# Kernel tuning notes

Hardware: AMD Instinct MI355X
Metric: run time of the kernel (lower is better)

## Reference

```python
import jax, jax.numpy as jnp
import numpy as np

B = 512; H = 84; W = 84; K = 20; DEPTH = 24; EMB = 512
FCS = 7 * 7 * 64
FLOW_C = 0.01


def _init(key, shape, fan_in):
    return jax.random.normal(key, shape, jnp.float32) * (1.0 / np.sqrt(fan_in))


def setup_inputs() -> dict:
    key = jax.random.key(0)
    ks = jax.random.split(key, 22)
    return {
        "inp": jax.random.normal(ks[0], (B, 2, H, W), jnp.float32),
        "cw1": _init(ks[1], (32, 2, 8, 8), 2 * 8 * 8),
        "cb1": jnp.zeros((32,), jnp.float32),
        "cw2": _init(ks[2], (64, 32, 4, 4), 32 * 4 * 4),
        "cb2": jnp.zeros((64,), jnp.float32),
        "cw3": _init(ks[3], (64, 64, 3, 3), 64 * 3 * 3),
        "cb3": jnp.zeros((64,), jnp.float32),
        "fcw": _init(ks[4], (EMB, FCS), FCS),
        "fcb": jnp.zeros((EMB,), jnp.float32),
        "otw": _init(ks[5], (K * 2, EMB), EMB),
        "otb": jnp.zeros((K * 2,), jnp.float32),
        "ctw": _init(ks[6], (2, EMB), EMB),
        "ctb": jnp.zeros((2,), jnp.float32),
        "m1w": _init(ks[7], (21 * 21 * DEPTH, EMB), EMB),
        "m1b": jnp.zeros((21 * 21 * DEPTH,), jnp.float32),
        "c1w": _init(ks[8], (DEPTH, DEPTH, 3, 3), DEPTH * 9),
        "c1b": jnp.zeros((DEPTH,), jnp.float32),
        "c2w": _init(ks[9], (DEPTH, DEPTH, 3, 3), DEPTH * 9),
        "c2b": jnp.zeros((DEPTH,), jnp.float32),
        "c3w": _init(ks[10], (K, DEPTH, 1, 1), DEPTH),
        "c3b": jnp.zeros((K,), jnp.float32),
    }


def _conv(x, w, b, stride, pad):
    y = jax.lax.conv_general_dilated(
        x, w, (stride, stride), [(pad, pad), (pad, pad)],
        dimension_numbers=("NCHW", "OIHW", "NCHW"))
    return y + b[None, :, None, None]


def _up_mat(in_s, out_s):
    # bilinear, align_corners=True (torch UpsamplingBilinear2d)
    pos = jnp.arange(out_s, dtype=jnp.float32) * ((in_s - 1) / (out_s - 1))
    lo = jnp.clip(jnp.floor(pos).astype(jnp.int32), 0, in_s - 2)
    w = pos - lo.astype(jnp.float32)
    r = jnp.arange(out_s)
    M = jnp.zeros((out_s, in_s), jnp.float32)
    M = M.at[r, lo].add(1.0 - w).at[r, lo + 1].add(w)
    return M


def reference(inp, cw1, cb1, cw2, cb2, cw3, cb3, fcw, fcb, otw, otb,
              ctw, ctb, m1w, m1b, c1w, c1b, c2w, c2b, c3w, c3b):
    bs = inp.shape[0]
    # CNN encoder
    h1 = jax.nn.relu(_conv(inp, cw1, cb1, 4, 0))
    h2 = jax.nn.relu(_conv(h1, cw2, cb2, 2, 0))
    h3 = jax.nn.relu(_conv(h2, cw3, cb3, 1, 0))
    feat = h3.reshape(bs, -1)                              # [B, 3136]
    x = jax.nn.relu(feat @ fcw.T + fcb)                    # [B, EMB]
    # mask decoder
    m = (x @ m1w.T + m1b).reshape(bs, DEPTH, 21, 21)
    M42 = _up_mat(21, 42)
    m = jnp.einsum('bchw,Hh,Ww->bcHW', m, M42, M42)        # 21->42
    m = jax.nn.relu(m + _conv(m, c1w, c1b, 1, 1))
    M84 = _up_mat(42, 84)
    m = jnp.einsum('bchw,Hh,Ww->bcHW', m, M84, M84)        # 42->84
    m = jax.nn.relu(m + _conv(m, c2w, c2b, 1, 1))
    m = jax.nn.sigmoid(_conv(m, c3w, c3b, 1, 0))           # [B, K, 84, 84]
    # per-object translations -> flow
    ot = (x @ otw.T + otb).reshape(bs, K, 2)
    flow = jnp.einsum('bkhw,bkt->bthw', m, ot).reshape(bs, 2, H * W)
    ct = (x @ ctw.T + ctb)[:, :, None]                     # [B,2,1]
    flat_flow = flow + ct
    img_size_f = FLOW_C * jnp.array([[float(H)], [float(W)]], jnp.float32)
    # mesh grid: row 0 = y (row index), row 1 = x (col index)
    gy = jnp.repeat(jnp.arange(H, dtype=jnp.float32), W)
    gx = jnp.tile(jnp.arange(W, dtype=jnp.float32), H)
    grid = jnp.stack([gy, gx], 0)                          # [2, H*W]
    coords = img_size_f * flat_flow + grid
    ys = coords[:, 0, :].reshape(-1)                       # [B*H*W]
    xs = coords[:, 1, :].reshape(-1)
    # manual bilinear gather from second input frame
    src = inp[:, 1, :, :].reshape(-1)                      # [B*H*W] flat image
    x0 = jnp.clip(jnp.floor(xs).astype(jnp.int32), 0, W - 1)
    x1 = jnp.clip(x0 + 1, 0, W - 1)
    y0 = jnp.clip(jnp.floor(ys).astype(jnp.int32), 0, H - 1)
    y1 = jnp.clip(y0 + 1, 0, H - 1)
    base = jnp.repeat(jnp.arange(bs, dtype=jnp.int32) * (H * W), H * W)
    Ia = src[base + y0 * W + x0]
    Ib = src[base + y1 * W + x0]
    Ic = src[base + y0 * W + x1]
    Id = src[base + y1 * W + x1]
    xc = jnp.clip(xs, 0.0, float(W - 1))
    yc = jnp.clip(ys, 0.0, float(H - 1))
    x0f = x0.astype(jnp.float32); x1f = x1.astype(jnp.float32)
    y0f = y0.astype(jnp.float32); y1f = y1.astype(jnp.float32)
    out = ((x1f - xc) * (y1f - yc) * Ia + (x1f - xc) * (yc - y0f) * Ib +
           (xc - x0f) * (y1f - yc) * Ic + (xc - x0f) * (yc - y0f) * Id)
    return out.reshape(bs, 1, H, W)
```

## Files before the change

kernel.cpp:

```cpp
#include <hip/hip_runtime.h>
#include <math.h>

namespace {

typedef float f32x2 __attribute__((ext_vector_type(2)));

#if defined(__has_builtin)
#if __has_builtin(__builtin_elementwise_fma)
#define HAVE_EW_FMA 1
#endif
#endif

__device__ __forceinline__ f32x2 pkfma(f32x2 a, f32x2 b, f32x2 c) {
#ifdef HAVE_EW_FMA
  return __builtin_elementwise_fma(a, b, c);
#else
  return a * b + c;
#endif
}

constexpr int IMS  = 84;
constexpr int NPIX = IMS * IMS;
constexpr int KOBJ = 20;

constexpr size_t OFF_X    = 0;
constexpr size_t OFF_OT   = 262144;
constexpr size_t OFF_CT   = 282624;
constexpr size_t OFF_WT2  = 283648;
constexpr size_t OFF_WT3  = 316416;
constexpr size_t OFF_M0   = 353280;
constexpr size_t OFF_R1   = 5772288;
constexpr size_t OFF_H1   = OFF_R1;
constexpr size_t OFF_H2   = 12325888;
constexpr size_t OFF_FEAT = 14980096;

__global__ void transpose_w(const float* __restrict__ w, float* __restrict__ wt,
                            int OC, int CKK) {
  int idx = blockIdx.x * 256 + threadIdx.x;
  if (idx < OC * CKK) {
    int oc = idx / CKK, ckk = idx % CKK;
    wt[ckk * OC + oc] = w[idx];
  }
}

__global__ __launch_bounds__(256) void conv1_k(
    const float* __restrict__ inp, const float* __restrict__ w,
    const float* __restrict__ bias, float* __restrict__ out) {
  __shared__ __align__(16) float sIn[NPIX];
  __shared__ __align__(16) float sW[128 * 32];
  const int b = blockIdx.x, t = threadIdx.x;
  for (int i = t; i < 4096; i += 256) {
    int oc = i >> 7, ckk = i & 127;
    sW[ckk * 32 + oc] = w[i];
  }
  const float* ip = inp + (size_t)b * 2 * NPIX;
  const int oc0 = (t & 7) * 4;
  const int pg  = t >> 3;
  int ibase[13];
#pragma unroll
  for (int k = 0; k < 13; k++) {
    int p = pg + 32 * k; if (p > 399) p = 399;
    ibase[k] = (p / 20) * 4 * 84 + (p % 20) * 4;
  }
  f32x2 acc[13][2];
#pragma unroll
  for (int k = 0; k < 13; k++) { acc[k][0] = f32x2{0.f, 0.f}; acc[k][1] = f32x2{0.f, 0.f}; }
  for (int c = 0; c < 2; c++) {
    __syncthreads();
    for (int i = t; i < NPIX; i += 256) sIn[i] = ip[c * NPIX + i];
    __syncthreads();
    for (int u = 0; u < 8; u++) {
#pragma unroll
      for (int v = 0; v < 8; v++) {
        const float4 wv = *(const float4*)&sW[((c * 8 + u) * 8 + v) * 32 + oc0];
        const f32x2 w0 = {wv.x, wv.y}, w1 = {wv.z, wv.w};
        const int off = u * 84 + v;
#pragma unroll
        for (int k = 0; k < 13; k++) {
          float x = sIn[off + ibase[k]];
          f32x2 xv = {x, x};
          acc[k][0] = pkfma(w0, xv, acc[k][0]);
          acc[k][1] = pkfma(w1, xv, acc[k][1]);
        }
      }
    }
  }
  float b0 = bias[oc0], b1 = bias[oc0+1], b2 = bias[oc0+2], b3 = bias[oc0+3];
  float* op = out + (size_t)b * 32 * 400;
#pragma unroll
  for (int k = 0; k < 13; k++) {
    int p = pg + 32 * k;
    if (p < 400) {
      op[(oc0+0)*400 + p] = fmaxf(acc[k][0][0] + b0, 0.f);
      op[(oc0+1)*400 + p] = fmaxf(acc[k][0][1] + b1, 0.f);
      op[(oc0+2)*400 + p] = fmaxf(acc[k][1][0] + b2, 0.f);
      op[(oc0+3)*400 + p] = fmaxf(acc[k][1][1] + b3, 0.f);
    }
  }
}

__global__ __launch_bounds__(256) void conv2_k(
    const float* __restrict__ in, const float* __restrict__ wt,
    const float* __restrict__ bias, float* __restrict__ out) {
  __shared__ float sIn[32 * 400];
  const int b = blockIdx.x, t = threadIdx.x;
  const float* ip = in + (size_t)b * 12800;
  for (int i = t; i < 12800; i += 256) sIn[i] = ip[i];
  __syncthreads();
  const int oc0 = (t & 7) * 8;
  const int pg  = t >> 3;
  int base[3];
#pragma unroll
  for (int k = 0; k < 3; k++) {
    int p = pg + 32 * k; if (p > 80) p = 80;
    base[k] = (p / 9) * 40 + (p % 9) * 2;
  }
  f32x2 acc[3][4];
#pragma unroll
  for (int k = 0; k < 3; k++)
#pragma unroll
    for (int o = 0; o < 4; o++) acc[k][o] = f32x2{0.f, 0.f};
  for (int c = 0; c < 32; c++) {
#pragma unroll
    for (int u = 0; u < 4; u++)
#pragma unroll
      for (int v = 0; v < 4; v++) {
        const float* wp = wt + ((c * 4 + u) * 4 + v) * 64 + oc0;
        float4 wa = *(const float4*)wp;
        float4 wb = *(const float4*)(wp + 4);
        const f32x2 w0 = {wa.x, wa.y}, w1 = {wa.z, wa.w};
        const f32x2 w2 = {wb.x, wb.y}, w3 = {wb.z, wb.w};
        int off = c * 400 + u * 20 + v;
#pragma unroll
        for (int k = 0; k < 3; k++) {
          float x = sIn[off + base[k]];
          f32x2 xv = {x, x};
          acc[k][0] = pkfma(w0, xv, acc[k][0]);
          acc[k][1] = pkfma(w1, xv, acc[k][1]);
          acc[k][2] = pkfma(w2, xv, acc[k][2]);
          acc[k][3] = pkfma(w3, xv, acc[k][3]);
        }
      }
  }
  float* op = out + (size_t)b * 5184;
#pragma unroll
  for (int k = 0; k < 3; k++) {
    int p = pg + 32 * k;
    if (p < 81) {
#pragma unroll
      for (int o = 0; o < 8; o++)
        op[(oc0+o)*81 + p] = fmaxf(acc[k][o >> 1][o & 1] + bias[oc0+o], 0.f);
    }
  }
}

__global__ __launch_bounds__(256) void conv3_k(
    const float* __restrict__ in, const float* __restrict__ wt,
    const float* __restrict__ bias, float* __restrict__ out) {
  __shared__ float sIn[64 * 81];
  const int b = blockIdx.x, t = threadIdx.x;
  const float* ip = in + (size_t)b * 5184;
  for (int i = t; i < 5184; i += 256) sIn[i] = ip[i];
  __syncthreads();
  const int oc0 = (t & 7) * 8;
  const int pg  = t >> 3;
  int base[2];
#pragma unroll
  for (int k = 0; k < 2; k++) {
    int p = pg + 32 * k; if (p > 48) p = 48;
    base[k] = (p / 7) * 9 + (p % 7);
  }
  f32x2 acc[2][4];
#pragma unroll
  for (int k = 0; k < 2; k++)
#pragma unroll
    for (int o = 0; o < 4; o++) acc[k][o] = f32x2{0.f, 0.f};
  for (int c = 0; c < 64; c++) {
#pragma unroll
    for (int u = 0; u < 3; u++)
#pragma unroll
      for (int v = 0; v < 3; v++) {
        const float* wp = wt + ((c * 3 + u) * 3 + v) * 64 + oc0;
        float4 wa = *(const float4*)wp;
        float4 wb = *(const float4*)(wp + 4);
        const f32x2 w0 = {wa.x, wa.y}, w1 = {wa.z, wa.w};
        const f32x2 w2 = {wb.x, wb.y}, w3 = {wb.z, wb.w};
        int off = c * 81 + u * 9 + v;
#pragma unroll
        for (int k = 0; k < 2; k++) {
          float x = sIn[off + base[k]];
          f32x2 xv = {x, x};
          acc[k][0] = pkfma(w0, xv, acc[k][0]);
          acc[k][1] = pkfma(w1, xv, acc[k][1]);
          acc[k][2] = pkfma(w2, xv, acc[k][2]);
          acc[k][3] = pkfma(w3, xv, acc[k][3]);
        }
      }
  }
  float* op = out + (size_t)b * 3136;
#pragma unroll
  for (int k = 0; k < 2; k++) {
    int p = pg + 32 * k;
    if (p < 49) {
#pragma unroll
      for (int o = 0; o < 8; o++)
        op[(oc0+o)*49 + p] = fmaxf(acc[k][o >> 1][o & 1] + bias[oc0+o], 0.f);
    }
  }
}

template<bool RELU>
__global__ __launch_bounds__(256) void gemm_k(
    const float* __restrict__ A, const float* __restrict__ Wm,
    const float* __restrict__ bias, float* __restrict__ C,
    int N, int K) {
  __shared__ __align__(16) float As[16][68];
  __shared__ __align__(16) float Ws[16][68];
  const int t = threadIdx.x;
  const int m0 = blockIdx.y * 64, n0 = blockIdx.x * 64;
  const int r  = t >> 2;
  const int kq = (t & 3) * 4;
  const int r0 = (t >> 4) * 4, c0 = (t & 15) * 4;
  f32x2 acc[4][2];
#pragma unroll
  for (int i = 0; i < 4; i++) { acc[i][0] = f32x2{0.f, 0.f}; acc[i][1] = f32x2{0.f, 0.f}; }
  for (int k0 = 0; k0 < K; k0 += 16) {
    float4 a = *(const float4*)(A + (size_t)(m0 + r) * K + k0 + kq);
    int wrow = n0 + r;
    float4 wv = make_float4(0.f, 0.f, 0.f, 0.f);
    if (wrow < N) wv = *(const float4*)(Wm + (size_t)wrow * K + k0 + kq);
    __syncthreads();
    As[kq+0][r] = a.x; As[kq+1][r] = a.y; As[kq+2][r] = a.z; As[kq+3][r] = a.w;
    Ws[kq+0][r] = wv.x; Ws[kq+1][r] = wv.y; Ws[kq+2][r] = wv.z; Ws[kq+3][r] = wv.w;
    __syncthreads();
#pragma unroll
    for (int kk = 0; kk < 16; kk++) {
      float4 av = *(const float4*)&As[kk][r0];
      float4 bv = *(const float4*)&Ws[kk][c0];
      const f32x2 b0 = {bv.x, bv.y}, b1 = {bv.z, bv.w};
      float ar[4] = {av.x, av.y, av.z, av.w};
#pragma unroll
      for (int i = 0; i < 4; i++) {
        f32x2 ai = {ar[i], ar[i]};
        acc[i][0] = pkfma(b0, ai, acc[i][0]);
        acc[i][1] = pkfma(b1, ai, acc[i][1]);
      }
    }
  }
#pragma unroll
  for (int i = 0; i < 4; i++) {
    int row = m0 + r0 + i;
#pragma unroll
    for (int j = 0; j < 4; j++) {
      int col = n0 + c0 + j;
      if (col < N) {
        float v = acc[i][j >> 1][j & 1] + bias[col];
        C[(size_t)row * N + col] = RELU ? fmaxf(v, 0.f) : v;
      }
    }
  }
}

__global__ __launch_bounds__(256, 4) void upconv1_k(
    const float* __restrict__ X, const float* __restrict__ wt,
    const float* __restrict__ bias, float* __restrict__ out) {
  constexpr int S_IN = 21, S_OUT = 42, TR = 6, UH = 8, UW = 44, NTILE = 7;
  __shared__ __align__(16) float sU[24 * UH * UW];
  const int b = blockIdx.x / NTILE;
  const int y0 = (blockIdx.x % NTILE) * TR;
  const int t = threadIdx.x;
  const float* xb = X + (size_t)b * 24 * S_IN * S_IN;
  const float sc = (float)(S_IN - 1) / (float)(S_OUT - 1);
  for (int rr = t; rr < UH * UW; rr += 256) {
    const int ry = rr / UW, cx = rr % UW;
    const int y = y0 + ry - 1, x = cx - 1;
    float* sdst = &sU[rr];
    if (y >= 0 && y < S_OUT && x >= 0 && x < S_OUT) {
      float py = y * sc, px = x * sc;
      int ly = (int)py; if (ly > S_IN - 2) ly = S_IN - 2;
      int lx = (int)px; if (lx > S_IN - 2) lx = S_IN - 2;
      float wy = py - (float)ly, wx = px - (float)lx;
      const f32x2 wxv = {wx, wx};
      const float* xc = xb + ly * S_IN + lx;
      for (int c = 0; c < 24; c++) {
        f32x2 a  = {xc[0], xc[S_IN]};
        f32x2 bb = {xc[1], xc[S_IN + 1]};
        f32x2 h = pkfma(wxv, bb - a, a);
        *sdst = h[0] + wy * (h[1] - h[0]);
        xc += S_IN * S_IN;
        sdst += UH * UW;
      }
    } else {
      for (int c = 0; c < 24; c++) { *sdst = 0.f; sdst += UH * UW; }
    }
  }
  __syncthreads();
  if (t < 252) {
    const int ry = t / 42, lx = t % 42;
    f32x2 acc[12];
#pragma unroll
    for (int j = 0; j < 12; j++) acc[j] = f32x2{0.f, 0.f};
    for (int ic = 0; ic < 24; ic++) {
      const float* urow = &sU[(ic * UH + ry) * UW + lx];
      const float* wp = wt + ic * 216;
#pragma unroll
      for (int ky = 0; ky < 3; ky++) {
        float x0v = urow[ky * UW + 0];
        float x1v = urow[ky * UW + 1];
        float x2v = urow[ky * UW + 2];
        f32x2 X0 = {x0v, x0v}, X1 = {x1v, x1v}, X2 = {x2v, x2v};
        const f32x2* wk2 = (const f32x2*)(wp + ky * 72);
#pragma unroll
        for (int j = 0; j < 12; j++)
          acc[j] = pkfma(wk2[j], X0,
                   pkfma(wk2[12 + j], X1,
                   pkfma(wk2[24 + j], X2, acc[j])));
      }
    }
    const int yy = y0 + ry;
#pragma unroll
    for (int j = 0; j < 12; j++) {
      f32x2 u2 = { sU[((2*j)   * UH + ry + 1) * UW + lx + 1],
                   sU[((2*j+1) * UH + ry + 1) * UW + lx + 1] };
      f32x2 b2 = *(const f32x2*)&bias[2*j];
      f32x2 s = u2 + acc[j] + b2;
      out[(((size_t)b * 24 + 2*j    ) * S_OUT + yy) * S_OUT + lx] = fmaxf(s[0], 0.f);
      out[(((size_t)b * 24 + 2*j + 1) * S_OUT + yy) * S_OUT + lx] = fmaxf(s[1], 0.f);
    }
  }
}

__global__ __launch_bounds__(256, 4) void upconv2_final_k(
    const float* __restrict__ R1, const float* __restrict__ inp,
    const float* __restrict__ wt, const float* __restrict__ bias,
    const float* __restrict__ c3w, const float* __restrict__ c3b,
    const float* __restrict__ ot, const float* __restrict__ ct,
    float* __restrict__ out) {
  constexpr int S_IN = 42, S_OUT = 84, TR = 6, UH = 8, TW = 42, UW = 44;
  __shared__ __align__(16) float sU[24 * UH * UW];
  const int blk = blockIdx.x;
  const int b = blk / 28;
  const int rr0 = blk % 28;
  const int y0 = (rr0 >> 1) * TR;
  const int x0 = (rr0 & 1) * TW;
  const int t = threadIdx.x;
  const float* xb = R1 + (size_t)b * 24 * S_IN * S_IN;
  const float sc = (float)(S_IN - 1) / (float)(S_OUT - 1);
  for (int rr = t; rr < UH * UW; rr += 256) {
    const int ry = rr / UW, cx = rr % UW;
    const int y = y0 + ry - 1, x = x0 + cx - 1;
    float* sdst = &sU[rr];
    if (y >= 0 && y < S_OUT && x >= 0 && x < S_OUT) {
      float py = y * sc, px = x * sc;
      int ly = (int)py; if (ly > S_IN - 2) ly = S_IN - 2;
      int lx = (int)px; if (lx > S_IN - 2) lx = S_IN - 2;
      float wy = py - (float)ly, wx = px - (float)lx;
      const f32x2 wxv = {wx, wx};
      const float* xc = xb + ly * S_IN + lx;
      for (int c = 0; c < 24; c++) {
        f32x2 a  = {xc[0], xc[S_IN]};
        f32x2 bb = {xc[1], xc[S_IN + 1]};
        f32x2 h = pkfma(wxv, bb - a, a);
        *sdst = h[0] + wy * (h[1] - h[0]);
        xc += S_IN * S_IN;
        sdst += UH * UW;
      }
    } else {
      for (int c = 0; c < 24; c++) { *sdst = 0.f; sdst += UH * UW; }
    }
  }
  __syncthreads();
  if (t < 252) {
    const int ry = t / 42, lx = t % 42;
    f32x2 acc[12];
#pragma unroll
    for (int j = 0; j < 12; j++) acc[j] = f32x2{0.f, 0.f};
    for (int ic = 0; ic < 24; ic++) {
      const float* urow = &sU[(ic * UH + ry) * UW + lx];
      const float* wp = wt + ic * 216;
#pragma unroll
      for (int ky = 0; ky < 3; ky++) {
        float x0v = urow[ky * UW + 0];
        float x1v = urow[ky * UW + 1];
        float x2v = urow[ky * UW + 2];
        f32x2 X0 = {x0v, x0v}, X1 = {x1v, x1v}, X2 = {x2v, x2v};
        const f32x2* wk2 = (const f32x2*)(wp + ky * 72);
#pragma unroll
        for (int j = 0; j < 12; j++)
          acc[j] = pkfma(wk2[j], X0,
                   pkfma(wk2[12 + j], X1,
                   pkfma(wk2[24 + j], X2, acc[j])));
      }
    }
    f32x2 r[12];
#pragma unroll
    for (int j = 0; j < 12; j++) {
      f32x2 u2 = { sU[((2*j)   * UH + ry + 1) * UW + lx + 1],
                   sU[((2*j+1) * UH + ry + 1) * UW + lx + 1] };
      f32x2 b2 = *(const f32x2*)&bias[2*j];
      f32x2 s = u2 + acc[j] + b2;
      r[j][0] = fmaxf(s[0], 0.f);
      r[j][1] = fmaxf(s[1], 0.f);
    }
    f32x2 f2 = *(const f32x2*)&ct[b * 2];
    const f32x2* ot2 = (const f32x2*)(ot + b * 2 * KOBJ);
    for (int k = 0; k < KOBJ; k++) {
      f32x2 zv = {c3b[k], 0.f};
      const f32x2* cw2 = (const f32x2*)(c3w + k * 24);
#pragma unroll
      for (int j = 0; j < 12; j++) zv = pkfma(r[j], cw2[j], zv);
      float z = zv[0] + zv[1];
      float m = 1.f / (1.f + __expf(-z));
      f32x2 mv = {m, m};
      f2 = pkfma(mv, ot2[k], f2);
    }
    const int gy = y0 + ry, gx = x0 + lx;
    const float imgf = 0.01f * 84.0f;
    float ys = imgf * f2[0] + (float)gy;
    float xs = imgf * f2[1] + (float)gx;
    int ix0 = (int)floorf(xs); ix0 = ix0 < 0 ? 0 : (ix0 > 83 ? 83 : ix0);
    int iy0 = (int)floorf(ys); iy0 = iy0 < 0 ? 0 : (iy0 > 83 ? 83 : iy0);
    int ix1 = ix0 + 1 > 83 ? 83 : ix0 + 1;
    int iy1 = iy0 + 1 > 83 ? 83 : iy0 + 1;
    float xc = fminf(fmaxf(xs, 0.f), 83.f);
    float yc = fminf(fmaxf(ys, 0.f), 83.f);
    float wx1 = (float)ix1 - xc, wx0 = xc - (float)ix0;
    float wy1 = (float)iy1 - yc, wy0 = yc - (float)iy0;
    const float* src = inp + ((size_t)b * 2 + 1) * NPIX;
    float Ia = src[iy0 * 84 + ix0], Ib = src[iy1 * 84 + ix0];
    float Ic = src[iy0 * 84 + ix1], Id = src[iy1 * 84 + ix1];
    out[(size_t)b * NPIX + gy * 84 + gx] =
        wx1 * wy1 * Ia + wx1 * wy0 * Ib + wx0 * wy1 * Ic + wx0 * wy0 * Id;
  }
}

}

extern "C" void kernel_launch(void* const* d_in, const int* in_sizes, int n_in,
                              void* d_out, int out_size, void* d_ws, size_t ws_size,
                              hipStream_t stream) {
  const float* inp = (const float*)d_in[0];
  const float* cw1 = (const float*)d_in[1];
  const float* cb1 = (const float*)d_in[2];
  const float* cw2 = (const float*)d_in[3];
  const float* cb2 = (const float*)d_in[4];
  const float* cw3 = (const float*)d_in[5];
  const float* cb3 = (const float*)d_in[6];
  const float* fcw = (const float*)d_in[7];
  const float* fcb = (const float*)d_in[8];
  const float* otw = (const float*)d_in[9];
  const float* otb = (const float*)d_in[10];
  const float* ctw = (const float*)d_in[11];
  const float* ctb = (const float*)d_in[12];
  const float* m1w = (const float*)d_in[13];
  const float* m1b = (const float*)d_in[14];
  const float* c1w = (const float*)d_in[15];
  const float* c1b = (const float*)d_in[16];
  const float* c2w = (const float*)d_in[17];
  const float* c2b = (const float*)d_in[18];
  const float* c3w = (const float*)d_in[19];
  const float* c3b = (const float*)d_in[20];
  float* W = (float*)d_ws;
  float* out = (float*)d_out;

  transpose_w<<<(64 * 512 + 255) / 256, 256, 0, stream>>>(cw2, W + OFF_WT2, 64, 512);
  transpose_w<<<(64 * 576 + 255) / 256, 256, 0, stream>>>(cw3, W + OFF_WT3, 64, 576);
  conv1_k<<<512, 256, 0, stream>>>(inp, cw1, cb1, W + OFF_H1);
  conv2_k<<<512, 256, 0, stream>>>(W + OFF_H1, W + OFF_WT2, cb2, W + OFF_H2);
  conv3_k<<<512, 256, 0, stream>>>(W + OFF_H2, W + OFF_WT3, cb3, W + OFF_FEAT);
  transpose_w<<<(24 * 216 + 255) / 256, 256, 0, stream>>>(c1w, W + OFF_WT2, 24, 216);
  transpose_w<<<(24 * 216 + 255) / 256, 256, 0, stream>>>(c2w, W + OFF_WT3, 24, 216);
  gemm_k<true><<<dim3(8, 8), 256, 0, stream>>>(W + OFF_FEAT, fcw, fcb, W + OFF_X, 512, 3136);
  gemm_k<false><<<dim3(1, 8), 256, 0, stream>>>(W + OFF_X, otw, otb, W + OFF_OT, 40, 512);
  gemm_k<false><<<dim3(1, 8), 256, 0, stream>>>(W + OFF_X, ctw, ctb, W + OFF_CT, 2, 512);
  gemm_k<false><<<dim3(166, 8), 256, 0, stream>>>(W + OFF_X, m1w, m1b, W + OFF_M0, 10584, 512);
  upconv1_k<<<512 * 7, 256, 0, stream>>>(W + OFF_M0, W + OFF_WT2, c1b, W + OFF_R1);
  upconv2_final_k<<<512 * 28, 256, 0, stream>>>(W + OFF_R1, inp, W + OFF_WT3, c2b,
                                                c3w, c3b, W + OFF_OT, W + OFF_CT, out);
}
```

Baseline: 1.204 ms.

## Use channel-interleaved shared layout in decoder convs and a 128x128 GEMM tile

```diff
diff --git a/kernel.cpp b/kernel.cpp
--- a/kernel.cpp
+++ b/kernel.cpp
@@ -40,6 +40,14 @@
   if (idx < OC * CKK) {
     int oc = idx / CKK, ckk = idx % CKK;
     wt[ckk * OC + oc] = w[idx];
+  }
+}
+
+__global__ void transpose_dec(const float* __restrict__ w, float* __restrict__ wt) {
+  int idx = blockIdx.x * 256 + threadIdx.x;
+  if (idx < 5184) {
+    int oc = idx / 216, rem = idx % 216, ic = rem / 9, tap = rem % 9;
+    wt[(tap * 24 + ic) * 24 + oc] = w[idx];
   }
 }
 
@@ -261,11 +269,73 @@
   }
 }
 
+__global__ __launch_bounds__(256) void gemm128_k(
+    const float* __restrict__ A, const float* __restrict__ Wm,
+    const float* __restrict__ bias, float* __restrict__ C,
+    int N, int K) {
+  __shared__ __align__(16) float As[16][132];
+  __shared__ __align__(16) float Ws[16][132];
+  const int t = threadIdx.x;
+  const int m0 = blockIdx.y * 128, n0 = blockIdx.x * 128;
+  const int lr = t >> 1;
+  const int kq = (t & 1) * 8;
+  const int r0 = (t >> 4) * 8, c0 = (t & 15) * 8;
+  f32x2 acc[8][4];
+#pragma unroll
+  for (int i = 0; i < 8; i++)
+#pragma unroll
+    for (int j = 0; j < 4; j++) acc[i][j] = f32x2{0.f, 0.f};
+  for (int k0 = 0; k0 < K; k0 += 16) {
+    const float* ap = A + (size_t)(m0 + lr) * K + k0 + kq;
+    float4 a0 = *(const float4*)ap;
+    float4 a1 = *(const float4*)(ap + 4);
+    int wrow = n0 + lr;
+    float4 w0 = make_float4(0.f,0.f,0.f,0.f), w1 = make_float4(0.f,0.f,0.f,0.f);
+    if (wrow < N) {
+      const float* wp = Wm + (size_t)wrow * K + k0 + kq;
+      w0 = *(const float4*)wp;
+      w1 = *(const float4*)(wp + 4);
+    }
+    __syncthreads();
+    As[kq+0][lr] = a0.x; As[kq+1][lr] = a0.y; As[kq+2][lr] = a0.z; As[kq+3][lr] = a0.w;
+    As[kq+4][lr] = a1.x; As[kq+5][lr] = a1.y; As[kq+6][lr] = a1.z; As[kq+7][lr] = a1.w;
+    Ws[kq+0][lr] = w0.x; Ws[kq+1][lr] = w0.y; Ws[kq+2][lr] = w0.z; Ws[kq+3][lr] = w0.w;
+    Ws[kq+4][lr] = w1.x; Ws[kq+5][lr] = w1.y; Ws[kq+6][lr] = w1.z; Ws[kq+7][lr] = w1.w;
+    __syncthreads();
+#pragma unroll
+    for (int kk = 0; kk < 16; kk++) {
+      float4 av0 = *(const float4*)&As[kk][r0];
+      float4 av1 = *(const float4*)&As[kk][r0 + 4];
+      float4 bv0 = *(const float4*)&Ws[kk][c0];
+      float4 bv1 = *(const float4*)&Ws[kk][c0 + 4];
+      float ar[8] = {av0.x, av0.y, av0.z, av0.w, av1.x, av1.y, av1.z, av1.w};
+      f32x2 br[4] = {{bv0.x, bv0.y}, {bv0.z, bv0.w}, {bv1.x, bv1.y}, {bv1.z, bv1.w}};
+#pragma unroll
+      for (int i = 0; i < 8; i++) {
+        f32x2 ai = {ar[i], ar[i]};
+#pragma unroll
+        for (int j = 0; j < 4; j++) acc[i][j] = pkfma(br[j], ai, acc[i][j]);
+      }
+    }
+  }
+#pragma unroll
+  for (int i = 0; i < 8; i++) {
+    int row = m0 + r0 + i;
+#pragma unroll
+    for (int j = 0; j < 8; j++) {
+      int col = n0 + c0 + j;
+      if (col < N)
+        C[(size_t)row * N + col] = acc[i][j >> 1][j & 1] + bias[col];
+    }
+  }
+}
+
 __global__ __launch_bounds__(256, 4) void upconv1_k(
     const float* __restrict__ X, const float* __restrict__ wt,
     const float* __restrict__ bias, float* __restrict__ out) {
   constexpr int S_IN = 21, S_OUT = 42, TR = 6, UH = 8, UW = 44, NTILE = 7;
-  __shared__ __align__(16) float sU[24 * UH * UW];
+  constexpr int CST = 28;
+  __shared__ __align__(16) float sU[UH * UW * CST];
   const int b = blockIdx.x / NTILE;
   const int y0 = (blockIdx.x % NTILE) * TR;
   const int t = threadIdx.x;
@@ -274,7 +344,7 @@
   for (int rr = t; rr < UH * UW; rr += 256) {
     const int ry = rr / UW, cx = rr % UW;
     const int y = y0 + ry - 1, x = cx - 1;
-    float* sdst = &sU[rr];
+    float vals[24];
     if (y >= 0 && y < S_OUT && x >= 0 && x < S_OUT) {
       float py = y * sc, px = x * sc;
       int ly = (int)py; if (ly > S_IN - 2) ly = S_IN - 2;
@@ -286,13 +356,17 @@
         f32x2 a  = {xc[0], xc[S_IN]};
         f32x2 bb = {xc[1], xc[S_IN + 1]};
         f32x2 h = pkfma(wxv, bb - a, a);
-        *sdst = h[0] + wy * (h[1] - h[0]);
+        vals[c] = h[0] + wy * (h[1] - h[0]);
         xc += S_IN * S_IN;
-        sdst += UH * UW;
       }
     } else {
-      for (int c = 0; c < 24; c++) { *sdst = 0.f; sdst += UH * UW; }
-    }
+#pragma unroll
+      for (int c = 0; c < 24; c++) vals[c] = 0.f;
+    }
+    float4* wd = (float4*)&sU[rr * CST];
+#pragma unroll
+    for (int w = 0; w < 6; w++)
+      wd[w] = make_float4(vals[4*w], vals[4*w+1], vals[4*w+2], vals[4*w+3]);
   }
   __syncthreads();
   if (t < 252) {
@@ -300,32 +374,35 @@
     f32x2 acc[12];
 #pragma unroll
     for (int j = 0; j < 12; j++) acc[j] = f32x2{0.f, 0.f};
-    for (int ic = 0; ic < 24; ic++) {
-      const float* urow = &sU[(ic * UH + ry) * UW + lx];
-      const float* wp = wt + ic * 216;
-#pragma unroll
-      for (int ky = 0; ky < 3; ky++) {
-        float x0v = urow[ky * UW + 0];
-        float x1v = urow[ky * UW + 1];
-        float x2v = urow[ky * UW + 2];
-        f32x2 X0 = {x0v, x0v}, X1 = {x1v, x1v}, X2 = {x2v, x2v};
-        const f32x2* wk2 = (const f32x2*)(wp + ky * 72);
-#pragma unroll
-        for (int j = 0; j < 12; j++)
-          acc[j] = pkfma(wk2[j], X0,
-                   pkfma(wk2[12 + j], X1,
-                   pkfma(wk2[24 + j], X2, acc[j])));
-      }
-    }
+    for (int ky = 0; ky < 3; ky++) {
+      for (int kx = 0; kx < 3; kx++) {
+        const float4* vp = (const float4*)&sU[((ry + ky) * UW + lx + kx) * CST];
+        float4 q[6];
+#pragma unroll
+        for (int w = 0; w < 6; w++) q[w] = vp[w];
+        const float* vin = (const float*)q;
+        const f32x2* w2 = (const f32x2*)(wt + (ky * 3 + kx) * 576);
+#pragma unroll
+        for (int ic = 0; ic < 24; ic++) {
+          f32x2 xv = {vin[ic], vin[ic]};
+#pragma unroll
+          for (int j = 0; j < 12; j++)
+            acc[j] = pkfma(w2[ic * 12 + j], xv, acc[j]);
+        }
+      }
+    }
+    const float4* cp = (const float4*)&sU[((ry + 1) * UW + lx + 1) * CST];
+    float4 cq[6];
+#pragma unroll
+    for (int w = 0; w < 6; w++) cq[w] = cp[w];
+    const float* cv = (const float*)cq;
     const int yy = y0 + ry;
 #pragma unroll
     for (int j = 0; j < 12; j++) {
-      f32x2 u2 = { sU[((2*j)   * UH + ry + 1) * UW + lx + 1],
-                   sU[((2*j+1) * UH + ry + 1) * UW + lx + 1] };
-      f32x2 b2 = *(const f32x2*)&bias[2*j];
-      f32x2 s = u2 + acc[j] + b2;
-      out[(((size_t)b * 24 + 2*j    ) * S_OUT + yy) * S_OUT + lx] = fmaxf(s[0], 0.f);
-      out[(((size_t)b * 24 + 2*j + 1) * S_OUT + yy) * S_OUT + lx] = fmaxf(s[1], 0.f);
+      float s0 = cv[2*j]     + acc[j][0] + bias[2*j];
+      float s1 = cv[2*j + 1] + acc[j][1] + bias[2*j + 1];
+      out[(((size_t)b * 24 + 2*j    ) * S_OUT + yy) * S_OUT + lx] = fmaxf(s0, 0.f);
+      out[(((size_t)b * 24 + 2*j + 1) * S_OUT + yy) * S_OUT + lx] = fmaxf(s1, 0.f);
     }
   }
 }
@@ -337,7 +414,8 @@
     const float* __restrict__ ot, const float* __restrict__ ct,
     float* __restrict__ out) {
   constexpr int S_IN = 42, S_OUT = 84, TR = 6, UH = 8, TW = 42, UW = 44;
-  __shared__ __align__(16) float sU[24 * UH * UW];
+  constexpr int CST = 28;
+  __shared__ __align__(16) float sU[UH * UW * CST];
   const int blk = blockIdx.x;
   const int b = blk / 28;
   const int rr0 = blk % 28;
@@ -349,7 +427,7 @@
   for (int rr = t; rr < UH * UW; rr += 256) {
     const int ry = rr / UW, cx = rr % UW;
     const int y = y0 + ry - 1, x = x0 + cx - 1;
-    float* sdst = &sU[rr];
+    float vals[24];
     if (y >= 0 && y < S_OUT && x >= 0 && x < S_OUT) {
       float py = y * sc, px = x * sc;
       int ly = (int)py; if (ly > S_IN - 2) ly = S_IN - 2;
@@ -361,13 +439,17 @@
         f32x2 a  = {xc[0], xc[S_IN]};
         f32x2 bb = {xc[1], xc[S_IN + 1]};
         f32x2 h = pkfma(wxv, bb - a, a);
-        *sdst = h[0] + wy * (h[1] - h[0]);
+        vals[c] = h[0] + wy * (h[1] - h[0]);
         xc += S_IN * S_IN;
-        sdst += UH * UW;
       }
     } else {
-      for (int c = 0; c < 24; c++) { *sdst = 0.f; sdst += UH * UW; }
-    }
+#pragma unroll
+      for (int c = 0; c < 24; c++) vals[c] = 0.f;
+    }
+    float4* wd = (float4*)&sU[rr * CST];
+#pragma unroll
+    for (int w = 0; w < 6; w++)
+      wd[w] = make_float4(vals[4*w], vals[4*w+1], vals[4*w+2], vals[4*w+3]);
   }
   __syncthreads();
   if (t < 252) {
@@ -375,32 +457,33 @@
     f32x2 acc[12];
 #pragma unroll
     for (int j = 0; j < 12; j++) acc[j] = f32x2{0.f, 0.f};
-    for (int ic = 0; ic < 24; ic++) {
-      const float* urow = &sU[(ic * UH + ry) * UW + lx];
-      const float* wp = wt + ic * 216;
-#pragma unroll
-      for (int ky = 0; ky < 3; ky++) {
-        float x0v = urow[ky * UW + 0];
-        float x1v = urow[ky * UW + 1];
-        float x2v = urow[ky * UW + 2];
-        f32x2 X0 = {x0v, x0v}, X1 = {x1v, x1v}, X2 = {x2v, x2v};
-        const f32x2* wk2 = (const f32x2*)(wp + ky * 72);
-#pragma unroll
-        for (int j = 0; j < 12; j++)
-          acc[j] = pkfma(wk2[j], X0,
-                   pkfma(wk2[12 + j], X1,
-                   pkfma(wk2[24 + j], X2, acc[j])));
-      }
-    }
+    for (int ky = 0; ky < 3; ky++) {
+      for (int kx = 0; kx < 3; kx++) {
+        const float4* vp = (const float4*)&sU[((ry + ky) * UW + lx + kx) * CST];
+        float4 q[6];
+#pragma unroll
+        for (int w = 0; w < 6; w++) q[w] = vp[w];
+        const float* vin = (const float*)q;
+        const f32x2* w2 = (const f32x2*)(wt + (ky * 3 + kx) * 576);
+#pragma unroll
+        for (int ic = 0; ic < 24; ic++) {
+          f32x2 xv = {vin[ic], vin[ic]};
+#pragma unroll
+          for (int j = 0; j < 12; j++)
+            acc[j] = pkfma(w2[ic * 12 + j], xv, acc[j]);
+        }
+      }
+    }
+    const float4* cp = (const float4*)&sU[((ry + 1) * UW + lx + 1) * CST];
+    float4 cq[6];
+#pragma unroll
+    for (int w = 0; w < 6; w++) cq[w] = cp[w];
+    const float* cv = (const float*)cq;
     f32x2 r[12];
 #pragma unroll
     for (int j = 0; j < 12; j++) {
-      f32x2 u2 = { sU[((2*j)   * UH + ry + 1) * UW + lx + 1],
-                   sU[((2*j+1) * UH + ry + 1) * UW + lx + 1] };
-      f32x2 b2 = *(const f32x2*)&bias[2*j];
-      f32x2 s = u2 + acc[j] + b2;
-      r[j][0] = fmaxf(s[0], 0.f);
-      r[j][1] = fmaxf(s[1], 0.f);
+      r[j][0] = fmaxf(cv[2*j]     + acc[j][0] + bias[2*j],     0.f);
+      r[j][1] = fmaxf(cv[2*j + 1] + acc[j][1] + bias[2*j + 1], 0.f);
     }
     f32x2 f2 = *(const f32x2*)&ct[b * 2];
     const f32x2* ot2 = (const f32x2*)(ot + b * 2 * KOBJ);
@@ -468,12 +551,12 @@
   conv1_k<<<512, 256, 0, stream>>>(inp, cw1, cb1, W + OFF_H1);
   conv2_k<<<512, 256, 0, stream>>>(W + OFF_H1, W + OFF_WT2, cb2, W + OFF_H2);
   conv3_k<<<512, 256, 0, stream>>>(W + OFF_H2, W + OFF_WT3, cb3, W + OFF_FEAT);
-  transpose_w<<<(24 * 216 + 255) / 256, 256, 0, stream>>>(c1w, W + OFF_WT2, 24, 216);
-  transpose_w<<<(24 * 216 + 255) / 256, 256, 0, stream>>>(c2w, W + OFF_WT3, 24, 216);
+  transpose_dec<<<(5184 + 255) / 256, 256, 0, stream>>>(c1w, W + OFF_WT2);
+  transpose_dec<<<(5184 + 255) / 256, 256, 0, stream>>>(c2w, W + OFF_WT3);
   gemm_k<true><<<dim3(8, 8), 256, 0, stream>>>(W + OFF_FEAT, fcw, fcb, W + OFF_X, 512, 3136);
   gemm_k<false><<<dim3(1, 8), 256, 0, stream>>>(W + OFF_X, otw, otb, W + OFF_OT, 40, 512);
   gemm_k<false><<<dim3(1, 8), 256, 0, stream>>>(W + OFF_X, ctw, ctb, W + OFF_CT, 2, 512);
-  gemm_k<false><<<dim3(166, 8), 256, 0, stream>>>(W + OFF_X, m1w, m1b, W + OFF_M0, 10584, 512);
+  gemm128_k<<<dim3(83, 4), 256, 0, stream>>>(W + OFF_X, m1w, m1b, W + OFF_M0, 10584, 512);
   upconv1_k<<<512 * 7, 256, 0, stream>>>(W + OFF_M0, W + OFF_WT2, c1b, W + OFF_R1);
   upconv2_final_k<<<512 * 28, 256, 0, stream>>>(W + OFF_R1, inp, W + OFF_WT3, c2b,
                                                 c3w, c3b, W + OFF_OT, W + OFF_CT, out);
```

After: 1.334 ms. 10.8% more time.

## Split-K the FC GEMM, use 128x128 tiles for m1 GEMM, widen upconv blocks

Applied to the files above, without the earlier changes.

```diff
diff --git a/kernel.cpp b/kernel.cpp
--- a/kernel.cpp
+++ b/kernel.cpp
@@ -261,7 +261,134 @@
   }
 }
 
-__global__ __launch_bounds__(256, 4) void upconv1_k(
+__global__ __launch_bounds__(256) void gemm_splitk_k(
+    const float* __restrict__ A, const float* __restrict__ Wm,
+    float* __restrict__ Cpart, int N, int K, int Kslice) {
+  __shared__ __align__(16) float As[16][68];
+  __shared__ __align__(16) float Ws[16][68];
+  const int t = threadIdx.x;
+  const int m0 = blockIdx.y * 64, n0 = blockIdx.x * 64;
+  const int kbeg = blockIdx.z * Kslice;
+  const int kend = kbeg + Kslice;
+  const int r  = t >> 2;
+  const int kq = (t & 3) * 4;
+  const int r0 = (t >> 4) * 4, c0 = (t & 15) * 4;
+  f32x2 acc[4][2];
+#pragma unroll
+  for (int i = 0; i < 4; i++) { acc[i][0] = f32x2{0.f, 0.f}; acc[i][1] = f32x2{0.f, 0.f}; }
+  for (int k0 = kbeg; k0 < kend; k0 += 16) {
+    float4 a = *(const float4*)(A + (size_t)(m0 + r) * K + k0 + kq);
+    float4 wv = *(const float4*)(Wm + (size_t)(n0 + r) * K + k0 + kq);
+    __syncthreads();
+    As[kq+0][r] = a.x; As[kq+1][r] = a.y; As[kq+2][r] = a.z; As[kq+3][r] = a.w;
+    Ws[kq+0][r] = wv.x; Ws[kq+1][r] = wv.y; Ws[kq+2][r] = wv.z; Ws[kq+3][r] = wv.w;
+    __syncthreads();
+#pragma unroll
+    for (int kk = 0; kk < 16; kk++) {
+      float4 av = *(const float4*)&As[kk][r0];
+      float4 bv = *(const float4*)&Ws[kk][c0];
+      const f32x2 b0 = {bv.x, bv.y}, b1 = {bv.z, bv.w};
+      float ar[4] = {av.x, av.y, av.z, av.w};
+#pragma unroll
+      for (int i = 0; i < 4; i++) {
+        f32x2 ai = {ar[i], ar[i]};
+        acc[i][0] = pkfma(b0, ai, acc[i][0]);
+        acc[i][1] = pkfma(b1, ai, acc[i][1]);
+      }
+    }
+  }
+  float* cp = Cpart + (size_t)blockIdx.z * 512 * 512;
+#pragma unroll
+  for (int i = 0; i < 4; i++) {
+    int row = m0 + r0 + i;
+#pragma unroll
+    for (int j = 0; j < 4; j++)
+      cp[(size_t)row * N + n0 + c0 + j] = acc[i][j >> 1][j & 1];
+  }
+}
+
+__global__ __launch_bounds__(256) void splitk_reduce_k(
+    const float* __restrict__ Cpart, const float* __restrict__ bias,
+    float* __restrict__ X) {
+  int i4 = blockIdx.x * 256 + threadIdx.x;
+  if (i4 < 65536) {
+    int col4 = (i4 & 127) * 4;
+    float4 p0 = *(const float4*)&Cpart[(size_t)i4 * 4];
+    float4 p1 = *(const float4*)&Cpart[262144 + (size_t)i4 * 4];
+    float4 p2 = *(const float4*)&Cpart[524288 + (size_t)i4 * 4];
+    float4 p3 = *(const float4*)&Cpart[786432 + (size_t)i4 * 4];
+    float4 bb = *(const float4*)&bias[col4];
+    float4 o;
+    o.x = fmaxf(p0.x + p1.x + p2.x + p3.x + bb.x, 0.f);
+    o.y = fmaxf(p0.y + p1.y + p2.y + p3.y + bb.y, 0.f);
+    o.z = fmaxf(p0.z + p1.z + p2.z + p3.z + bb.z, 0.f);
+    o.w = fmaxf(p0.w + p1.w + p2.w + p3.w + bb.w, 0.f);
+    *(float4*)&X[(size_t)i4 * 4] = o;
+  }
+}
+
+__global__ __launch_bounds__(256) void gemm128_k(
+    const float* __restrict__ A, const float* __restrict__ Wm,
+    const float* __restrict__ bias, float* __restrict__ C,
+    int N, int K) {
+  __shared__ __align__(16) float As[16][132];
+  __shared__ __align__(16) float Ws[16][132];
+  const int t = threadIdx.x;
+  const int m0 = blockIdx.y * 128, n0 = blockIdx.x * 128;
+  const int lr = t >> 1;
+  const int kq = (t & 1) * 8;
+  const int r0 = (t >> 4) * 8, c0 = (t & 15) * 8;
+  f32x2 acc[8][4];
+#pragma unroll
+  for (int i = 0; i < 8; i++)
+#pragma unroll
+    for (int j = 0; j < 4; j++) acc[i][j] = f32x2{0.f, 0.f};
+  for (int k0 = 0; k0 < K; k0 += 16) {
+    const float* ap = A + (size_t)(m0 + lr) * K + k0 + kq;
+    float4 a0 = *(const float4*)ap;
+    float4 a1 = *(const float4*)(ap + 4);
+    int wrow = n0 + lr;
+    float4 w0 = make_float4(0.f,0.f,0.f,0.f), w1 = make_float4(0.f,0.f,0.f,0.f);
+    if (wrow < N) {
+      const float* wp = Wm + (size_t)wrow * K + k0 + kq;
+      w0 = *(const float4*)wp;
+      w1 = *(const float4*)(wp + 4);
+    }
+    __syncthreads();
+    As[kq+0][lr] = a0.x; As[kq+1][lr] = a0.y; As[kq+2][lr] = a0.z; As[kq+3][lr] = a0.w;
+    As[kq+4][lr] = a1.x; As[kq+5][lr] = a1.y; As[kq+6][lr] = a1.z; As[kq+7][lr] = a1.w;
+    Ws[kq+0][lr] = w0.x; Ws[kq+1][lr] = w0.y; Ws[kq+2][lr] = w0.z; Ws[kq+3][lr] = w0.w;
+    Ws[kq+4][lr] = w1.x; Ws[kq+5][lr] = w1.y; Ws[kq+6][lr] = w1.z; Ws[kq+7][lr] = w1.w;
+    __syncthreads();
+#pragma unroll
+    for (int kk = 0; kk < 16; kk++) {
+      float4 av0 = *(const float4*)&As[kk][r0];
+      float4 av1 = *(const float4*)&As[kk][r0 + 4];
+      float4 bv0 = *(const float4*)&Ws[kk][c0];
+      float4 bv1 = *(const float4*)&Ws[kk][c0 + 4];
+      float ar[8] = {av0.x, av0.y, av0.z, av0.w, av1.x, av1.y, av1.z, av1.w};
+      f32x2 br[4] = {{bv0.x, bv0.y}, {bv0.z, bv0.w}, {bv1.x, bv1.y}, {bv1.z, bv1.w}};
+#pragma unroll
+      for (int i = 0; i < 8; i++) {
+        f32x2 ai = {ar[i], ar[i]};
+#pragma unroll
+        for (int j = 0; j < 4; j++) acc[i][j] = pkfma(br[j], ai, acc[i][j]);
+      }
+    }
+  }
+#pragma unroll
+  for (int i = 0; i < 8; i++) {
+    int row = m0 + r0 + i;
+#pragma unroll
+    for (int j = 0; j < 8; j++) {
+      int col = n0 + c0 + j;
+      if (col < N)
+        C[(size_t)row * N + col] = acc[i][j >> 1][j & 1] + bias[col];
+    }
+  }
+}
+
+__global__ __launch_bounds__(384, 6) void upconv1_k(
     const float* __restrict__ X, const float* __restrict__ wt,
     const float* __restrict__ bias, float* __restrict__ out) {
   constexpr int S_IN = 21, S_OUT = 42, TR = 6, UH = 8, UW = 44, NTILE = 7;
@@ -271,7 +398,7 @@
   const int t = threadIdx.x;
   const float* xb = X + (size_t)b * 24 * S_IN * S_IN;
   const float sc = (float)(S_IN - 1) / (float)(S_OUT - 1);
-  for (int rr = t; rr < UH * UW; rr += 256) {
+  for (int rr = t; rr < UH * UW; rr += 384) {
     const int ry = rr / UW, cx = rr % UW;
     const int y = y0 + ry - 1, x = cx - 1;
     float* sdst = &sU[rr];
@@ -330,7 +457,7 @@
   }
 }
 
-__global__ __launch_bounds__(256, 4) void upconv2_final_k(
+__global__ __launch_bounds__(384, 6) void upconv2_final_k(
     const float* __restrict__ R1, const float* __restrict__ inp,
     const float* __restrict__ wt, const float* __restrict__ bias,
     const float* __restrict__ c3w, const float* __restrict__ c3b,
@@ -346,7 +473,7 @@
   const int t = threadIdx.x;
   const float* xb = R1 + (size_t)b * 24 * S_IN * S_IN;
   const float sc = (float)(S_IN - 1) / (float)(S_OUT - 1);
-  for (int rr = t; rr < UH * UW; rr += 256) {
+  for (int rr = t; rr < UH * UW; rr += 384) {
     const int ry = rr / UW, cx = rr % UW;
     const int y = y0 + ry - 1, x = x0 + cx - 1;
     float* sdst = &sU[rr];
@@ -470,11 +597,13 @@
   conv3_k<<<512, 256, 0, stream>>>(W + OFF_H2, W + OFF_WT3, cb3, W + OFF_FEAT);
   transpose_w<<<(24 * 216 + 255) / 256, 256, 0, stream>>>(c1w, W + OFF_WT2, 24, 216);
   transpose_w<<<(24 * 216 + 255) / 256, 256, 0, stream>>>(c2w, W + OFF_WT3, 24, 216);
-  gemm_k<true><<<dim3(8, 8), 256, 0, stream>>>(W + OFF_FEAT, fcw, fcb, W + OFF_X, 512, 3136);
+  gemm_splitk_k<<<dim3(8, 8, 4), 256, 0, stream>>>(W + OFF_FEAT, fcw, W + OFF_M0,
+                                                   512, 3136, 784);
+  splitk_reduce_k<<<256, 256, 0, stream>>>(W + OFF_M0, fcb, W + OFF_X);
   gemm_k<false><<<dim3(1, 8), 256, 0, stream>>>(W + OFF_X, otw, otb, W + OFF_OT, 40, 512);
   gemm_k<false><<<dim3(1, 8), 256, 0, stream>>>(W + OFF_X, ctw, ctb, W + OFF_CT, 2, 512);
-  gemm_k<false><<<dim3(166, 8), 256, 0, stream>>>(W + OFF_X, m1w, m1b, W + OFF_M0, 10584, 512);
-  upconv1_k<<<512 * 7, 256, 0, stream>>>(W + OFF_M0, W + OFF_WT2, c1b, W + OFF_R1);
-  upconv2_final_k<<<512 * 28, 256, 0, stream>>>(W + OFF_R1, inp, W + OFF_WT3, c2b,
+  gemm128_k<<<dim3(83, 4), 256, 0, stream>>>(W + OFF_X, m1w, m1b, W + OFF_M0, 10584, 512);
+  upconv1_k<<<512 * 7, 384, 0, stream>>>(W + OFF_M0, W + OFF_WT2, c1b, W + OFF_R1);
+  upconv2_final_k<<<512 * 28, 384, 0, stream>>>(W + OFF_R1, inp, W + OFF_WT3, c2b,
                                                 c3w, c3b, W + OFF_OT, W + OFF_CT, out);
 }
```

After: 1.103 ms. -8.4%, faster.
